# Performance work log

Measured on AMD Instinct MI355X. Metric: run time of the kernel, lower is better.

The kernel has to match this reference:

```python
import jax, jax.numpy as jnp
import numpy as np

# Output volume shape passed as `shape` to forward_3stacks / interpol.grid_push
VOL_SHAPE = (128, 128, 128)


def _grid_push(inp, grid, out_shape):
    """Trilinear scatter-splat (interpol.grid_push, bound=replicate, extrapolate=True).

    inp:  [B, C, D, H, W] values
    grid: [B, D, H, W, 3] target coords in output voxel space, (z, y, x) order
    returns [B, C, *out_shape]
    """
    B, C = inp.shape[0], inp.shape[1]
    S0, S1, S2 = out_shape
    N = inp.shape[2] * inp.shape[3] * inp.shape[4]
    vals = inp.reshape(B, C, N)
    coords = grid.reshape(B, N, 3)

    def push_one(v, g):  # v: [C, N], g: [N, 3]
        g0f = jnp.floor(g)
        f = g - g0f                      # trilinear fractions, [N, 3]
        g0 = g0f.astype(jnp.int32)
        acc = jnp.zeros((C, S0 * S1 * S2), dtype=v.dtype)
        for dz in (0, 1):
            wz = f[:, 0] if dz else 1.0 - f[:, 0]
            iz = jnp.clip(g0[:, 0] + dz, 0, S0 - 1)
            for dy in (0, 1):
                wy = f[:, 1] if dy else 1.0 - f[:, 1]
                iy = jnp.clip(g0[:, 1] + dy, 0, S1 - 1)
                for dx in (0, 1):
                    wx = f[:, 2] if dx else 1.0 - f[:, 2]
                    ix = jnp.clip(g0[:, 2] + dx, 0, S2 - 1)
                    flat = (iz * S1 + iy) * S2 + ix  # [N]
                    w = (wz * wy * wx)[None, :]      # [1, N]
                    acc = acc.at[:, flat].add(v * w)
        return acc.reshape(C, S0, S1, S2)

    return jax.vmap(push_one)(vals, coords)


def setup_inputs() -> dict:
    key = jax.random.key(0)
    k1, k2, k3 = jax.random.split(key, 3)
    x = jax.random.normal(k1, (1, 1, 384, 128, 128), dtype=jnp.float32)
    flow = jax.random.normal(k2, (1, 3, 384, 128, 128), dtype=jnp.float32)
    mask = jax.random.uniform(k3, (1, 1, 384, 128, 128), dtype=jnp.float32)
    return {"x": x, "flow": flow, "mask": mask}


def reference(x, flow, mask):
    """WarpingLayer_3stacks.forward_3stacks with transpose=True, warp=True.

    flow already matches x's spatial shape, so the F.interpolate resize is identity
    (the branch `if flow.shape[2:] != x.shape[2:]` is not taken).
    """
    # per-dim flow rescale: flow[:, d-2] * (x.shape[d]-1)/(flow.shape[d]-1)
    scale = jnp.asarray([(x.shape[d] - 1) / (flow.shape[d] - 1) for d in range(2, 5)],
                        dtype=x.dtype)
    flow = flow * scale[None, :, None, None, None]

    D, H, W = x.shape[2], x.shape[3], x.shape[4]
    gz, gy, gx = jnp.meshgrid(jnp.arange(D, dtype=x.dtype),
                              jnp.arange(H, dtype=x.dtype),
                              jnp.arange(W, dtype=x.dtype), indexing='ij')
    base = jnp.stack([gz, gy, gx], axis=0)          # [3, D, H, W]
    grid = flow + base[None]                        # self.warp * flow + meshgrid
    grid = jnp.transpose(grid, (0, 2, 3, 4, 1))     # [B, D, H, W, 3]

    intensities = jnp.concatenate([x * mask, mask], axis=1)  # [B, 2, D, H, W]
    return _grid_push(intensities, grid, VOL_SHAPE)          # [B, 2, 128, 128, 128]
```

## Files before the change

kernel.cpp:

```cpp
#include <hip/hip_runtime.h>


#define OS    128
#define OS3   (OS * OS * OS)
#define SRC_D 384
#define SRC_H 128
#define SRC_W 128
#define NSRC  (SRC_D * SRC_H * SRC_W)
#define ZSPLIT 128
#define PLANE_CELLS (OS * OS)

#define TZ 8
#define TY 4
#define HALO 3
#define NJOBS 140
#define GITER 9
#define GBLK  512

#define PGROUPS 64
#define PSPB    4
#define PBLK    (PGROUPS * 4)

#define REG_CAP 1024
#define LCAP    65536

#define OFF_CNT    0
#define OFF_COUNTS 1024
#define OFF_REGS   8192
#define OFF_LIST   (OFF_REGS + GBLK * REG_CAP * 16)
#define OFF_PART   (16 * 1024 * 1024)
#define WS_NEED    (OFF_PART + PGROUPS * 2 * PLANE_CELLS * 4)

#define S_FIX   262144.0f
#define INV_FIX (1.0f / 262144.0f)

__device__ __forceinline__ unsigned long long packt(float a, float b) {
    int vi = (int)a;
    int mi = (int)b;
    return ((unsigned long long)(unsigned)vi << 32) | (unsigned long long)(unsigned)mi;
}

__device__ __forceinline__ int swzq(int c) { return c ^ ((c >> 4) & 7); }

__device__ __forceinline__ void atomAddF(float* p, float v) {
    unsafeAtomicAdd(p, v);
}

__global__ __launch_bounds__(512) void warp_fused(
    const float* __restrict__ x, const float* __restrict__ flow,
    const float* __restrict__ mask, float* __restrict__ out,
    float* __restrict__ partials,
    unsigned* __restrict__ gcnt, int* __restrict__ counts,
    int4* __restrict__ regs, int4* __restrict__ list)
{
    __shared__ unsigned long long sh[4096];
    __shared__ int scnt;

    const int tid = threadIdx.x;
    const int b = blockIdx.x;

    const float4* __restrict__ fz4 = (const float4*)flow;
    const float4* __restrict__ fy4 = (const float4*)(flow + NSRC);
    const float4* __restrict__ fx4 = (const float4*)(flow + 2 * NSRC);
    const float4* __restrict__ m4p = (const float4*)mask;
    const float4* __restrict__ x4p = (const float4*)x;

    if (b < GBLK) {
        if (tid == 0) scnt = 0;
        #pragma unroll
        for (int s = 0; s < 4096 / 512; ++s)
            sh[tid + s * 512] = 0ull;
        __syncthreads();

        const int z0 = (b & 15) * TZ;
        const int y0 = (b >> 4) * TY;
        const int wq = tid & 31;
        const int slot = tid >> 5;

        for (int it = 0; it < GITER; ++it) {
            int j = it * 16 + slot;
            int dz = j / 10, dyy = j - dz * 10;
            int zzr = z0 - HALO + dz;
            int hhr = y0 - HALO + dyy;
            int zz = min(max(zzr, 0), ZSPLIT - 1);
            int hh = min(max(hhr, 0), OS - 1);
            bool vrow = (j < NJOBS) && (zzr >= 0) && (zzr < ZSPLIT) &&
                        (hhr >= 0) && (hhr < OS);
            bool home = vrow && (zzr >= z0) && (zzr < z0 + TZ) &&
                        (hhr >= y0) && (hhr < y0 + TY);

            int idx4 = (((zz << 14) + (hh << 7)) >> 2) + wq;
            float4 vfz = fz4[idx4];
            float4 vfy = fy4[idx4];
            float4 vfx = fx4[idx4];
            float4 vm  = m4p[idx4];
            float4 vx  = x4p[idx4];

            if (!vrow) continue;

            #pragma unroll
            for (int p = 0; p < 4; ++p) {
                float gz = ((float*)&vfz)[p] + (float)zz;
                float gy = ((float*)&vfy)[p] + (float)hh;
                float fzf = floorf(gz), fyf = floorf(gy);
                float ffz = gz - fzf, ffy = gy - fyf;
                int iz0 = (int)fzf, iy0 = (int)fyf;

                int cz0 = min(max(iz0,     0), OS - 1);
                int cz1 = min(max(iz0 + 1, 0), OS - 1);
                int cy0 = min(max(iy0,     0), OS - 1);
                int cy1 = min(max(iy0 + 1, 0), OS - 1);

                bool zin = (cz1 >= z0) && (cz0 < z0 + TZ);
                bool yin = (cy1 >= y0) && (cy0 < y0 + TY);
                if (!home && !(zin && yin)) continue;

                int w = wq * 4 + p;
                float gx = ((float*)&vfx)[p] + (float)w;
                float fxf = floorf(gx);
                float ffx = gx - fxf;
                int ix0 = (int)fxf;
                int cx0 = min(max(ix0,     0), OS - 1);
                int cx1 = min(max(ix0 + 1, 0), OS - 1);

                float m = ((float*)&vm)[p];
                float v = ((float*)&vx)[p] * m;
                float v_s = v * S_FIX;
                float m_s = m * S_FIX;

                #pragma unroll
                for (int d2 = 0; d2 < 2; ++d2) {
                    int cz = d2 ? cz1 : cz0;
                    float wz = d2 ? ffz : 1.0f - ffz;
                    bool nz = (cz - zz <= HALO) && (zz - cz <= HALO);
                    int uz = cz - z0;
                    #pragma unroll
                    for (int e2 = 0; e2 < 2; ++e2) {
                        int cy = e2 ? cy1 : cy0;
                        float wzy = wz * (e2 ? ffy : 1.0f - ffy);
                        bool ny = (cy - hh <= HALO) && (hh - cy <= HALO);
                        int uy = cy - y0;
                        bool nearc = nz && ny;
                        #pragma unroll
                        for (int f2 = 0; f2 < 2; ++f2) {
                            int cx = f2 ? cx1 : cx0;
                            float wgt = wzy * (f2 ? ffx : 1.0f - ffx);
                            if (nearc) {
                                if ((unsigned)uz < TZ && (unsigned)uy < TY) {
                                    int off = ((uz * TY + uy) << 7) + swzq(cx);
                                    atomicAdd(&sh[off], packt(v_s * wgt, m_s * wgt));
                                }
                            } else if (home) {
                                int4 r;
                                r.x = (cz << 14) + (cy << 7) + cx;
                                r.y = __float_as_int(v * wgt);
                                r.z = __float_as_int(m * wgt);
                                r.w = 0;
                                int s = atomicAdd(&scnt, 1);
                                if (s < REG_CAP) regs[b * REG_CAP + s] = r;
                                else {
                                    unsigned g = atomicAdd(gcnt, 1u);
                                    if (g < LCAP) list[g] = r;
                                }
                            }
                        }
                    }
                }
            }
        }

        __syncthreads();
        if (tid == 0) counts[b] = min(scnt, REG_CAP);

        for (int i = tid; i < TZ * TY * OS; i += 512) {
            int row = i >> 7;
            int c   = i & 127;
            unsigned long long cell = sh[(row << 7) | swzq(c)];
            float v = (float)(int)(cell >> 32) * INV_FIX;
            float m = (float)(int)(unsigned)cell * INV_FIX;
            int uz = row >> 2, uy = row & 3;
            int o = ((z0 + uz) << 14) + ((y0 + uy) << 7) + c;
            out[o]       = v;
            out[OS3 + o] = m;
        }
    } else {
        const int pb = b - GBLK;
        const int g  = pb >> 2;
        const int q  = pb & 3;
        const int ybase = q << 5;
        const int rlo = max(0, ybase - 5);
        const int rhi = min(OS, ybase + 32 + 5);

        #pragma unroll
        for (int s = 0; s < 4096 / 512; ++s)
            sh[tid + s * 512] = 0ull;
        __syncthreads();

        const int wq = tid & 31;
        const int rs = tid >> 5;

        for (int s = 0; s < PSPB; ++s) {
            int z = ZSPLIT + g * PSPB + s;
            for (int rb = 0; rb < 3; ++rb) {
                int r = rlo + rb * 16 + rs;
                bool valid = r < rhi;
                int rc = min(r, OS - 1);
                int idx4 = (((z << 14) + (rc << 7)) >> 2) + wq;
                float4 vfz = fz4[idx4];
                float4 vfy = fy4[idx4];
                float4 vfx = fx4[idx4];
                float4 vm  = m4p[idx4];
                float4 vx  = x4p[idx4];
                if (!valid) continue;
                bool homeRow = ((r >> 5) == q);

                #pragma unroll
                for (int p = 0; p < 4; ++p) {
                    int w = wq * 4 + p;
                    float gz = ((float*)&vfz)[p] + (float)z;
                    float gy = ((float*)&vfy)[p] + (float)r;
                    float gx = ((float*)&vfx)[p] + (float)w;
                    float m  = ((float*)&vm)[p];
                    float v  = ((float*)&vx)[p] * m;

                    float fyf = floorf(gy), fxf = floorf(gx);
                    float ffy = gy - fyf, ffx = gx - fxf;
                    int iy0 = (int)fyf, ix0 = (int)fxf;
                    int cy0 = min(max(iy0,     0), OS - 1);
                    int cy1 = min(max(iy0 + 1, 0), OS - 1);
                    int cx0 = min(max(ix0,     0), OS - 1);
                    int cx1 = min(max(ix0 + 1, 0), OS - 1);
                    int sx0 = swzq(cx0), sx1 = swzq(cx1);

                    if (gz >= (float)(OS - 1)) {
                        float wy0 = 1.0f - ffy, wy1 = ffy;
                        float wx0 = 1.0f - ffx, wx1 = ffx;
                        float v_s = v * S_FIX;
                        float m_s = m * S_FIX;

                        int u0 = cy0 - ybase;
                        bool n0 = (cy0 - r <= 5) && (r - cy0 <= 5);
                        if (n0 && (unsigned)u0 < 32u) {
                            unsigned long long* row = &sh[u0 << 7];
                            float a = v_s * wy0, bb = m_s * wy0;
                            atomicAdd(&row[sx0], packt(a * wx0, bb * wx0));
                            atomicAdd(&row[sx1], packt(a * wx1, bb * wx1));
                        }
                        int u1 = cy1 - ybase;
                        bool n1 = (cy1 - r <= 5) && (r - cy1 <= 5);
                        if (n1 && (unsigned)u1 < 32u) {
                            unsigned long long* row = &sh[u1 << 7];
                            float a = v_s * wy1, bb = m_s * wy1;
                            atomicAdd(&row[sx0], packt(a * wx0, bb * wx0));
                            atomicAdd(&row[sx1], packt(a * wx1, bb * wx1));
                        }
                        if (homeRow && (!n0 || !n1)) {
                            const int pbase = (OS - 1) << 14;
                            #pragma unroll
                            for (int e2 = 0; e2 < 2; ++e2) {
                                bool far = e2 ? !n1 : !n0;
                                if (!far) continue;
                                int cy = e2 ? cy1 : cy0;
                                float wy = e2 ? wy1 : wy0;
                                unsigned base = atomicAdd(gcnt, 2u);
                                #pragma unroll
                                for (int f2 = 0; f2 < 2; ++f2) {
                                    unsigned slt = base + f2;
                                    if (slt < LCAP) {
                                        float wgt = wy * (f2 ? wx1 : wx0);
                                        int4 qq;
                                        qq.x = pbase + (cy << 7) + (f2 ? cx1 : cx0);
                                        qq.y = __float_as_int(v * wgt);
                                        qq.z = __float_as_int(m * wgt);
                                        qq.w = 0;
                                        list[slt] = qq;
                                    }
                                }
                            }
                        }
                    } else if (homeRow) {
                        float fzf = floorf(gz);
                        float ffz = gz - fzf;
                        int iz0 = (int)fzf;
                        unsigned base = atomicAdd(gcnt, 8u);
                        int t = 0;
                        #pragma unroll
                        for (int d2 = 0; d2 < 2; ++d2) {
                            int cz = min(max(iz0 + d2, 0), OS - 1);
                            float wz = d2 ? ffz : 1.0f - ffz;
                            #pragma unroll
                            for (int e2 = 0; e2 < 2; ++e2) {
                                int cy = e2 ? cy1 : cy0;
                                float wzy = wz * (e2 ? ffy : 1.0f - ffy);
                                #pragma unroll
                                for (int f2 = 0; f2 < 2; ++f2) {
                                    int cx = f2 ? cx1 : cx0;
                                    float wgt = wzy * (f2 ? ffx : 1.0f - ffx);
                                    unsigned slt = base + t;
                                    if (slt < LCAP) {
                                        int4 qq;
                                        qq.x = (cz << 14) + (cy << 7) + cx;
                                        qq.y = __float_as_int(v * wgt);
                                        qq.z = __float_as_int(m * wgt);
                                        qq.w = 0;
                                        list[slt] = qq;
                                    }
                                    ++t;
                                }
                            }
                        }
                    }
                }
            }
        }

        __syncthreads();

        float* dst0 = partials + (size_t)g * 2 * PLANE_CELLS;
        float* dst1 = dst0 + PLANE_CELLS;
        for (int i = tid; i < 32 * OS; i += 512) {
            int row = i >> 7, c = i & 127;
            unsigned long long cell = sh[(row << 7) | swzq(c)];
            float v = (float)(int)(cell >> 32) * INV_FIX;
            float m = (float)(int)(unsigned)cell * INV_FIX;
            int o = ((ybase + row) << 7) + c;
            dst0[o] = v;
            dst1[o] = m;
        }
    }
}

#define RBLK 128
__global__ __launch_bounds__(256) void finalize(
    float* __restrict__ out, const float* __restrict__ partials,
    const unsigned* __restrict__ gcnt, const int* __restrict__ counts,
    const int4* __restrict__ regs, const int4* __restrict__ list)
{
    int b = blockIdx.x;
    if (b < RBLK) {
        int t = b * 256 + threadIdx.x;
        int ch   = t >> 14;
        int cell = t & 16383;
        const float* p = partials + (size_t)ch * PLANE_CELLS + cell;
        float s = 0.0f;
        #pragma unroll 8
        for (int g = 0; g < PGROUPS; ++g)
            s += p[(size_t)g * 2 * PLANE_CELLS];
        atomAddF(out + ch * OS3 + ((OS - 1) << 14) + cell, s);
    } else if (b < RBLK + GBLK) {
        int rb = b - RBLK;
        int n = counts[rb];
        const int4* r = regs + (size_t)rb * REG_CAP;
        for (int i = threadIdx.x; i < n; i += 256) {
            int4 q = r[i];
            atomAddF(out + q.x,       __int_as_float(q.y));
            atomAddF(out + OS3 + q.x, __int_as_float(q.z));
        }
    } else {
        unsigned n = *gcnt;
        if (n > LCAP) n = LCAP;
        for (unsigned i = (unsigned)(b - RBLK - GBLK) * 256 + threadIdx.x;
             i < n; i += 8 * 256) {
            int4 q = list[i];
            atomAddF(out + q.x,       __int_as_float(q.y));
            atomAddF(out + OS3 + q.x, __int_as_float(q.z));
        }
    }
}

__global__ __launch_bounds__(256) void warp_push_naive(
    const float* __restrict__ x, const float* __restrict__ flow,
    const float* __restrict__ mask, float* __restrict__ out, int N)
{
    int idx = blockIdx.x * blockDim.x + threadIdx.x;
    if (idx >= N) return;
    int w = idx & 127, h = (idx >> 7) & 127, z = idx >> 14;
    float gz = flow[idx] + (float)z;
    float gy = flow[N + idx] + (float)h;
    float gx = flow[2 * N + idx] + (float)w;
    float m = mask[idx];
    float v0 = x[idx] * m;
    float fz0 = floorf(gz), fy0 = floorf(gy), fx0 = floorf(gx);
    float fz = gz - fz0, fy = gy - fy0, fx = gx - fx0;
    int iz0 = (int)fz0, iy0 = (int)fy0, ix0 = (int)fx0;
    #pragma unroll
    for (int dz = 0; dz < 2; ++dz) {
        int cz = min(max(iz0 + dz, 0), OS - 1);
        float wz = dz ? fz : 1.0f - fz;
        #pragma unroll
        for (int dy = 0; dy < 2; ++dy) {
            int cy = min(max(iy0 + dy, 0), OS - 1);
            float wzy = wz * (dy ? fy : 1.0f - fy);
            #pragma unroll
            for (int dx = 0; dx < 2; ++dx) {
                int cx = min(max(ix0 + dx, 0), OS - 1);
                float wgt = wzy * (dx ? fx : 1.0f - fx);
                int o = (cz << 14) + (cy << 7) + cx;
                atomAddF(out + o,       v0 * wgt);
                atomAddF(out + OS3 + o, m * wgt);
            }
        }
    }
}

extern "C" void kernel_launch(void* const* d_in, const int* in_sizes, int n_in,
                              void* d_out, int out_size, void* d_ws, size_t ws_size,
                              hipStream_t stream) {
    (void)in_sizes; (void)n_in; (void)out_size;
    const float* x    = (const float*)d_in[0];
    const float* flow = (const float*)d_in[1];
    const float* mask = (const float*)d_in[2];
    float* out = (float*)d_out;

    if (ws_size >= (size_t)WS_NEED) {
        char* wsb = (char*)d_ws;
        unsigned* gcnt = (unsigned*)(wsb + OFF_CNT);
        int* counts    = (int*)(wsb + OFF_COUNTS);
        int4* regs     = (int4*)(wsb + OFF_REGS);
        int4* list     = (int4*)(wsb + OFF_LIST);
        float* parts   = (float*)(wsb + OFF_PART);

        hipMemsetAsync(d_ws, 0, 64, stream);

        warp_fused<<<GBLK + PBLK, 512, 0, stream>>>(
            x, flow, mask, out, parts, gcnt, counts, regs, list);
        finalize<<<RBLK + GBLK + 8, 256, 0, stream>>>(
            out, parts, gcnt, counts, regs, list);
    } else {
        hipMemsetAsync(d_out, 0, (size_t)2 * OS3 * sizeof(float), stream);
        warp_push_naive<<<NSRC / 256, 256, 0, stream>>>(x, flow, mask, out, NSRC);
    }
}
```

Before: 189.6 us.

## Skip halo row loads early and double partial-plane groups

Measured after the change: 200.0 us. 5.5% more time.

```diff
diff --git a/kernel.cpp b/kernel.cpp
--- a/kernel.cpp
+++ b/kernel.cpp
@@ -17,8 +17,8 @@
 #define GITER 9
 #define GBLK  512
 
-#define PGROUPS 64
-#define PSPB    4
+#define PGROUPS 128
+#define PSPB    2
 #define PBLK    (PGROUPS * 4)
 
 #define REG_CAP 1024
@@ -28,7 +28,7 @@
 #define OFF_COUNTS 1024
 #define OFF_REGS   8192
 #define OFF_LIST   (OFF_REGS + GBLK * REG_CAP * 16)
-#define OFF_PART   (16 * 1024 * 1024)
+#define OFF_PART   (10 * 1024 * 1024)
 #define WS_NEED    (OFF_PART + PGROUPS * 2 * PLANE_CELLS * 4)
 
 #define S_FIX   262144.0f
@@ -46,7 +46,7 @@
     unsafeAtomicAdd(p, v);
 }
 
-__global__ __launch_bounds__(512) void warp_fused(
+__global__ __launch_bounds__(512, 8) void warp_fused(
     const float* __restrict__ x, const float* __restrict__ flow,
     const float* __restrict__ mask, float* __restrict__ out,
     float* __restrict__ partials,
@@ -76,6 +76,11 @@
         const int y0 = (b >> 4) * TY;
         const int wq = tid & 31;
         const int slot = tid >> 5;
+
+        const float ztlo = (z0 == 0)           ? -1e30f : (float)(z0 - 1);
+        const float zthi = (z0 + TZ == ZSPLIT) ?  1e30f : (float)(z0 + TZ);
+        const float ytlo = (y0 == 0)           ? -1e30f : (float)(y0 - 1);
+        const float ythi = (y0 + TY == OS)     ?  1e30f : (float)(y0 + TY);
 
         for (int it = 0; it < GITER; ++it) {
             int j = it * 16 + slot;
@@ -92,14 +97,28 @@
             int idx4 = (((zz << 14) + (hh << 7)) >> 2) + wq;
             float4 vfz = fz4[idx4];
             float4 vfy = fy4[idx4];
+            if (!vrow) continue;
+
+            int hitm = 15;
+            if (!home) {
+                hitm = 0;
+                #pragma unroll
+                for (int p = 0; p < 4; ++p) {
+                    float gz = ((float*)&vfz)[p] + (float)zz;
+                    float gy = ((float*)&vfy)[p] + (float)hh;
+                    if (gz >= ztlo && gz < zthi && gy >= ytlo && gy < ythi)
+                        hitm |= 1 << p;
+                }
+                if (hitm == 0) continue;
+            }
+
             float4 vfx = fx4[idx4];
             float4 vm  = m4p[idx4];
             float4 vx  = x4p[idx4];
 
-            if (!vrow) continue;
-
             #pragma unroll
             for (int p = 0; p < 4; ++p) {
+                if (!home && !((hitm >> p) & 1)) continue;
                 float gz = ((float*)&vfz)[p] + (float)zz;
                 float gy = ((float*)&vfy)[p] + (float)hh;
                 float fzf = floorf(gz), fyf = floorf(gy);
@@ -191,6 +210,9 @@
         const int rlo = max(0, ybase - 5);
         const int rhi = min(OS, ybase + 32 + 5);
 
+        const float pylo = (ybase == 0)       ? -1e30f : (float)(ybase - 1);
+        const float pyhi = (ybase + 32 == OS) ?  1e30f : (float)(ybase + 32);
+
         #pragma unroll
         for (int s = 0; s < 4096 / 512; ++s)
             sh[tid + s * 512] = 0ull;
@@ -206,16 +228,29 @@
                 bool valid = r < rhi;
                 int rc = min(r, OS - 1);
                 int idx4 = (((z << 14) + (rc << 7)) >> 2) + wq;
+                float4 vfy = fy4[idx4];
+                if (!valid) continue;
+                bool homeRow = ((r >> 5) == q);
+
+                int hitm = 15;
+                if (!homeRow) {
+                    hitm = 0;
+                    #pragma unroll
+                    for (int p = 0; p < 4; ++p) {
+                        float gy = ((float*)&vfy)[p] + (float)r;
+                        if (gy >= pylo && gy < pyhi) hitm |= 1 << p;
+                    }
+                    if (hitm == 0) continue;
+                }
+
                 float4 vfz = fz4[idx4];
-                float4 vfy = fy4[idx4];
                 float4 vfx = fx4[idx4];
                 float4 vm  = m4p[idx4];
                 float4 vx  = x4p[idx4];
-                if (!valid) continue;
-                bool homeRow = ((r >> 5) == q);
 
                 #pragma unroll
                 for (int p = 0; p < 4; ++p) {
+                    if (!((hitm >> p) & 1)) continue;
                     int w = wq * 4 + p;
                     float gz = ((float*)&vfz)[p] + (float)z;
                     float gy = ((float*)&vfy)[p] + (float)r;
```

## Shrink gather halo and software-prefetch next row loads in both phases

Applied to the files above, without the earlier changes.

Result: slower. 303.8 us (+60.3%).

```diff
diff --git a/kernel.cpp b/kernel.cpp
--- a/kernel.cpp
+++ b/kernel.cpp
@@ -12,16 +12,16 @@
 
 #define TZ 8
 #define TY 4
-#define HALO 3
-#define NJOBS 140
-#define GITER 9
+#define HALO 2
+#define NJOBS 96
+#define GITER 6
 #define GBLK  512
 
 #define PGROUPS 64
 #define PSPB    4
 #define PBLK    (PGROUPS * 4)
 
-#define REG_CAP 1024
+#define REG_CAP 1536
 #define LCAP    65536
 
 #define OFF_CNT    0
@@ -77,24 +77,44 @@
         const int wq = tid & 31;
         const int slot = tid >> 5;
 
-        for (int it = 0; it < GITER; ++it) {
-            int j = it * 16 + slot;
-            int dz = j / 10, dyy = j - dz * 10;
+        float4 nfz, nfy, nfx, nvm, nvx;
+        int nzz, nhh;
+        bool nvrow, nhome;
+        {
+            int j = slot;
+            int dz = j >> 3, dyy = j & 7;
             int zzr = z0 - HALO + dz;
             int hhr = y0 - HALO + dyy;
-            int zz = min(max(zzr, 0), ZSPLIT - 1);
-            int hh = min(max(hhr, 0), OS - 1);
-            bool vrow = (j < NJOBS) && (zzr >= 0) && (zzr < ZSPLIT) &&
+            nzz = min(max(zzr, 0), ZSPLIT - 1);
+            nhh = min(max(hhr, 0), OS - 1);
+            nvrow = (zzr >= 0) && (zzr < ZSPLIT) && (hhr >= 0) && (hhr < OS);
+            nhome = nvrow && (zzr >= z0) && (zzr < z0 + TZ) &&
+                    (hhr >= y0) && (hhr < y0 + TY);
+            int idx4 = (((nzz << 14) + (nhh << 7)) >> 2) + wq;
+            nfz = fz4[idx4]; nfy = fy4[idx4]; nfx = fx4[idx4];
+            nvm = m4p[idx4]; nvx = x4p[idx4];
+        }
+
+        for (int it = 0; it < GITER; ++it) {
+            float4 vfz = nfz, vfy = nfy, vfx = nfx, vm = nvm, vx = nvx;
+            const int zz = nzz, hh = nhh;
+            const bool vrow = nvrow, home = nhome;
+
+            {
+                int j = (it + 1) * 16 + slot;
+                int dz = j >> 3, dyy = j & 7;
+                int zzr = z0 - HALO + dz;
+                int hhr = y0 - HALO + dyy;
+                nzz = min(max(zzr, 0), ZSPLIT - 1);
+                nhh = min(max(hhr, 0), OS - 1);
+                nvrow = (j < NJOBS) && (zzr >= 0) && (zzr < ZSPLIT) &&
                         (hhr >= 0) && (hhr < OS);
-            bool home = vrow && (zzr >= z0) && (zzr < z0 + TZ) &&
+                nhome = nvrow && (zzr >= z0) && (zzr < z0 + TZ) &&
                         (hhr >= y0) && (hhr < y0 + TY);
-
-            int idx4 = (((zz << 14) + (hh << 7)) >> 2) + wq;
-            float4 vfz = fz4[idx4];
-            float4 vfy = fy4[idx4];
-            float4 vfx = fx4[idx4];
-            float4 vm  = m4p[idx4];
-            float4 vx  = x4p[idx4];
+                int idx4 = (((nzz << 14) + (nhh << 7)) >> 2) + wq;
+                nfz = fz4[idx4]; nfy = fy4[idx4]; nfx = fx4[idx4];
+                nvm = m4p[idx4]; nvx = x4p[idx4];
+            }
 
             if (!vrow) continue;
 
@@ -199,114 +219,133 @@
         const int wq = tid & 31;
         const int rs = tid >> 5;
 
-        for (int s = 0; s < PSPB; ++s) {
-            int z = ZSPLIT + g * PSPB + s;
-            for (int rb = 0; rb < 3; ++rb) {
-                int r = rlo + rb * 16 + rs;
-                bool valid = r < rhi;
-                int rc = min(r, OS - 1);
-                int idx4 = (((z << 14) + (rc << 7)) >> 2) + wq;
-                float4 vfz = fz4[idx4];
-                float4 vfy = fy4[idx4];
-                float4 vfx = fx4[idx4];
-                float4 vm  = m4p[idx4];
-                float4 vx  = x4p[idx4];
-                if (!valid) continue;
-                bool homeRow = ((r >> 5) == q);
-
-                #pragma unroll
-                for (int p = 0; p < 4; ++p) {
-                    int w = wq * 4 + p;
-                    float gz = ((float*)&vfz)[p] + (float)z;
-                    float gy = ((float*)&vfy)[p] + (float)r;
-                    float gx = ((float*)&vfx)[p] + (float)w;
-                    float m  = ((float*)&vm)[p];
-                    float v  = ((float*)&vx)[p] * m;
-
-                    float fyf = floorf(gy), fxf = floorf(gx);
-                    float ffy = gy - fyf, ffx = gx - fxf;
-                    int iy0 = (int)fyf, ix0 = (int)fxf;
-                    int cy0 = min(max(iy0,     0), OS - 1);
-                    int cy1 = min(max(iy0 + 1, 0), OS - 1);
-                    int cx0 = min(max(ix0,     0), OS - 1);
-                    int cx1 = min(max(ix0 + 1, 0), OS - 1);
-                    int sx0 = swzq(cx0), sx1 = swzq(cx1);
-
-                    if (gz >= (float)(OS - 1)) {
-                        float wy0 = 1.0f - ffy, wy1 = ffy;
-                        float wx0 = 1.0f - ffx, wx1 = ffx;
-                        float v_s = v * S_FIX;
-                        float m_s = m * S_FIX;
-
-                        int u0 = cy0 - ybase;
-                        bool n0 = (cy0 - r <= 5) && (r - cy0 <= 5);
-                        if (n0 && (unsigned)u0 < 32u) {
-                            unsigned long long* row = &sh[u0 << 7];
-                            float a = v_s * wy0, bb = m_s * wy0;
-                            atomicAdd(&row[sx0], packt(a * wx0, bb * wx0));
-                            atomicAdd(&row[sx1], packt(a * wx1, bb * wx1));
-                        }
-                        int u1 = cy1 - ybase;
-                        bool n1 = (cy1 - r <= 5) && (r - cy1 <= 5);
-                        if (n1 && (unsigned)u1 < 32u) {
-                            unsigned long long* row = &sh[u1 << 7];
-                            float a = v_s * wy1, bb = m_s * wy1;
-                            atomicAdd(&row[sx0], packt(a * wx0, bb * wx0));
-                            atomicAdd(&row[sx1], packt(a * wx1, bb * wx1));
-                        }
-                        if (homeRow && (!n0 || !n1)) {
-                            const int pbase = (OS - 1) << 14;
+        float4 nfz, nfy, nfx, nvm, nvx;
+        int nr, nz;
+        {
+            int r0 = rlo + rs;
+            int rc0 = min(r0, OS - 1);
+            int zp  = ZSPLIT + g * PSPB;
+            int idx4 = (((zp << 14) + (rc0 << 7)) >> 2) + wq;
+            nfz = fz4[idx4]; nfy = fy4[idx4]; nfx = fx4[idx4];
+            nvm = m4p[idx4]; nvx = x4p[idx4];
+            nr = r0; nz = zp;
+        }
+        int cs = 0, crb = 0;
+
+        for (int k = 0; k < PSPB * 3; ++k) {
+            float4 vfz = nfz, vfy = nfy, vfx = nfx, vm = nvm, vx = nvx;
+            const int r = nr;
+            const int z = nz;
+
+            {
+                int krb = (crb == 2) ? 0 : crb + 1;
+                int ks  = (crb == 2) ? cs + 1 : cs;
+                int rn  = rlo + krb * 16 + rs;
+                int zn  = min(ZSPLIT + g * PSPB + ks, SRC_D - 1);
+                int rcn = min(rn, OS - 1);
+                int idx4 = (((zn << 14) + (rcn << 7)) >> 2) + wq;
+                nfz = fz4[idx4]; nfy = fy4[idx4]; nfx = fx4[idx4];
+                nvm = m4p[idx4]; nvx = x4p[idx4];
+                nr = rn; nz = (ks < PSPB) ? zn : z;
+                cs = ks; crb = krb;
+            }
+
+            bool valid = r < rhi;
+            if (!valid) continue;
+            bool homeRow = ((r >> 5) == q);
+
+            #pragma unroll
+            for (int p = 0; p < 4; ++p) {
+                int w = wq * 4 + p;
+                float gz = ((float*)&vfz)[p] + (float)z;
+                float gy = ((float*)&vfy)[p] + (float)r;
+                float gx = ((float*)&vfx)[p] + (float)w;
+                float m  = ((float*)&vm)[p];
+                float v  = ((float*)&vx)[p] * m;
+
+                float fyf = floorf(gy), fxf = floorf(gx);
+                float ffy = gy - fyf, ffx = gx - fxf;
+                int iy0 = (int)fyf, ix0 = (int)fxf;
+                int cy0 = min(max(iy0,     0), OS - 1);
+                int cy1 = min(max(iy0 + 1, 0), OS - 1);
+                int cx0 = min(max(ix0,     0), OS - 1);
+                int cx1 = min(max(ix0 + 1, 0), OS - 1);
+                int sx0 = swzq(cx0), sx1 = swzq(cx1);
+
+                if (gz >= (float)(OS - 1)) {
+                    float wy0 = 1.0f - ffy, wy1 = ffy;
+                    float wx0 = 1.0f - ffx, wx1 = ffx;
+                    float v_s = v * S_FIX;
+                    float m_s = m * S_FIX;
+
+                    int u0 = cy0 - ybase;
+                    bool n0 = (cy0 - r <= 5) && (r - cy0 <= 5);
+                    if (n0 && (unsigned)u0 < 32u) {
+                        unsigned long long* row = &sh[u0 << 7];
+                        float a = v_s * wy0, bb = m_s * wy0;
+                        atomicAdd(&row[sx0], packt(a * wx0, bb * wx0));
+                        atomicAdd(&row[sx1], packt(a * wx1, bb * wx1));
+                    }
+                    int u1 = cy1 - ybase;
+                    bool n1 = (cy1 - r <= 5) && (r - cy1 <= 5);
+                    if (n1 && (unsigned)u1 < 32u) {
+                        unsigned long long* row = &sh[u1 << 7];
+                        float a = v_s * wy1, bb = m_s * wy1;
+                        atomicAdd(&row[sx0], packt(a * wx0, bb * wx0));
+                        atomicAdd(&row[sx1], packt(a * wx1, bb * wx1));
+                    }
+                    if (homeRow && (!n0 || !n1)) {
+                        const int pbase = (OS - 1) << 14;
+                        #pragma unroll
+                        for (int e2 = 0; e2 < 2; ++e2) {
+                            bool far = e2 ? !n1 : !n0;
+                            if (!far) continue;
+                            int cy = e2 ? cy1 : cy0;
+                            float wy = e2 ? wy1 : wy0;
+                            unsigned base = atomicAdd(gcnt, 2u);
                             #pragma unroll
-                            for (int e2 = 0; e2 < 2; ++e2) {
-                                bool far = e2 ? !n1 : !n0;
-                                if (!far) continue;
-                                int cy = e2 ? cy1 : cy0;
-                                float wy = e2 ? wy1 : wy0;
-                                unsigned base = atomicAdd(gcnt, 2u);
-                                #pragma unroll
-                                for (int f2 = 0; f2 < 2; ++f2) {
-                                    unsigned slt = base + f2;
-                                    if (slt < LCAP) {
-                                        float wgt = wy * (f2 ? wx1 : wx0);
-                                        int4 qq;
-                                        qq.x = pbase + (cy << 7) + (f2 ? cx1 : cx0);
-                                        qq.y = __float_as_int(v * wgt);
-                                        qq.z = __float_as_int(m * wgt);
-                                        qq.w = 0;
-                                        list[slt] = qq;
-                                    }
+                            for (int f2 = 0; f2 < 2; ++f2) {
+                                unsigned slt = base + f2;
+                                if (slt < LCAP) {
+                                    float wgt = wy * (f2 ? wx1 : wx0);
+                                    int4 qq;
+                                    qq.x = pbase + (cy << 7) + (f2 ? cx1 : cx0);
+                                    qq.y = __float_as_int(v * wgt);
+                                    qq.z = __float_as_int(m * wgt);
+                                    qq.w = 0;
+                                    list[slt] = qq;
                                 }
                             }
                         }
-                    } else if (homeRow) {
-                        float fzf = floorf(gz);
-                        float ffz = gz - fzf;
-                        int iz0 = (int)fzf;
-                        unsigned base = atomicAdd(gcnt, 8u);
-                        int t = 0;
+                    }
+                } else if (homeRow) {
+                    float fzf = floorf(gz);
+                    float ffz = gz - fzf;
+                    int iz0 = (int)fzf;
+                    unsigned base = atomicAdd(gcnt, 8u);
+                    int t = 0;
+                    #pragma unroll
+                    for (int d2 = 0; d2 < 2; ++d2) {
+                        int cz = min(max(iz0 + d2, 0), OS - 1);
+                        float wz = d2 ? ffz : 1.0f - ffz;
                         #pragma unroll
-                        for (int d2 = 0; d2 < 2; ++d2) {
-                            int cz = min(max(iz0 + d2, 0), OS - 1);
-                            float wz = d2 ? ffz : 1.0f - ffz;
+                        for (int e2 = 0; e2 < 2; ++e2) {
+                            int cy = e2 ? cy1 : cy0;
+                            float wzy = wz * (e2 ? ffy : 1.0f - ffy);
                             #pragma unroll
-                            for (int e2 = 0; e2 < 2; ++e2) {
-                                int cy = e2 ? cy1 : cy0;
-                                float wzy = wz * (e2 ? ffy : 1.0f - ffy);
-                                #pragma unroll
-                                for (int f2 = 0; f2 < 2; ++f2) {
-                                    int cx = f2 ? cx1 : cx0;
-                                    float wgt = wzy * (f2 ? ffx : 1.0f - ffx);
-                                    unsigned slt = base + t;
-                                    if (slt < LCAP) {
-                                        int4 qq;
-                                        qq.x = (cz << 14) + (cy << 7) + cx;
-                                        qq.y = __float_as_int(v * wgt);
-                                        qq.z = __float_as_int(m * wgt);
-                                        qq.w = 0;
-                                        list[slt] = qq;
-                                    }
-                                    ++t;
+                            for (int f2 = 0; f2 < 2; ++f2) {
+                                int cx = f2 ? cx1 : cx0;
+                                float wgt = wzy * (f2 ? ffx : 1.0f - ffx);
+                                unsigned slt = base + t;
+                                if (slt < LCAP) {
+                                    int4 qq;
+                                    qq.x = (cz << 14) + (cy << 7) + cx;
+                                    qq.y = __float_as_int(v * wgt);
+                                    qq.z = __float_as_int(m * wgt);
+                                    qq.w = 0;
+                                    list[slt] = qq;
                                 }
+                                ++t;
                             }
                         }
                     }
```

## Enlarge scatter tiles to 8x8 rows, prefetch next row, use global region counters

Applied to the files above, without the earlier changes.

Measured after the change: 221.1 us. +16.6%, slower.

```diff
diff --git a/kernel.cpp b/kernel.cpp
--- a/kernel.cpp
+++ b/kernel.cpp
@@ -11,11 +11,11 @@
 #define PLANE_CELLS (OS * OS)
 
 #define TZ 8
-#define TY 4
+#define TY 8
 #define HALO 3
-#define NJOBS 140
-#define GITER 9
-#define GBLK  512
+#define NJOBS 196
+#define GITER 13
+#define GBLK  256
 
 #define PGROUPS 64
 #define PSPB    4
@@ -53,9 +53,7 @@
     unsigned* __restrict__ gcnt, int* __restrict__ counts,
     int4* __restrict__ regs, int4* __restrict__ list)
 {
-    __shared__ unsigned long long sh[4096];
-    __shared__ int scnt;
-
+    __shared__ unsigned long long sh[8192];
     const int tid = threadIdx.x;
     const int b = blockIdx.x;
 
@@ -66,9 +64,8 @@
     const float4* __restrict__ x4p = (const float4*)x;
 
     if (b < GBLK) {
-        if (tid == 0) scnt = 0;
         #pragma unroll
-        for (int s = 0; s < 4096 / 512; ++s)
+        for (int s = 0; s < 8192 / 512; ++s)
             sh[tid + s * 512] = 0ull;
         __syncthreads();
 
@@ -77,24 +74,44 @@
         const int wq = tid & 31;
         const int slot = tid >> 5;
 
-        for (int it = 0; it < GITER; ++it) {
-            int j = it * 16 + slot;
-            int dz = j / 10, dyy = j - dz * 10;
+        float4 nfz, nfy, nfx, nvm, nvx;
+        int nzz, nhh;
+        bool nvrow, nhome;
+        {
+            int j = slot;
+            int dz = j / 14, dyy = j - dz * 14;
             int zzr = z0 - HALO + dz;
             int hhr = y0 - HALO + dyy;
-            int zz = min(max(zzr, 0), ZSPLIT - 1);
-            int hh = min(max(hhr, 0), OS - 1);
-            bool vrow = (j < NJOBS) && (zzr >= 0) && (zzr < ZSPLIT) &&
+            nzz = min(max(zzr, 0), ZSPLIT - 1);
+            nhh = min(max(hhr, 0), OS - 1);
+            nvrow = (zzr >= 0) && (zzr < ZSPLIT) && (hhr >= 0) && (hhr < OS);
+            nhome = nvrow && (zzr >= z0) && (zzr < z0 + TZ) &&
+                    (hhr >= y0) && (hhr < y0 + TY);
+            int idx4 = (((nzz << 14) + (nhh << 7)) >> 2) + wq;
+            nfz = fz4[idx4]; nfy = fy4[idx4]; nfx = fx4[idx4];
+            nvm = m4p[idx4]; nvx = x4p[idx4];
+        }
+
+        for (int it = 0; it < GITER; ++it) {
+            float4 vfz = nfz, vfy = nfy, vfx = nfx, vm = nvm, vx = nvx;
+            const int zz = nzz, hh = nhh;
+            const bool vrow = nvrow, home = nhome;
+
+            {
+                int j = (it + 1) * 16 + slot;
+                int dz = j / 14, dyy = j - dz * 14;
+                int zzr = z0 - HALO + dz;
+                int hhr = y0 - HALO + dyy;
+                nzz = min(max(zzr, 0), ZSPLIT - 1);
+                nhh = min(max(hhr, 0), OS - 1);
+                nvrow = (j < NJOBS) && (zzr >= 0) && (zzr < ZSPLIT) &&
                         (hhr >= 0) && (hhr < OS);
-            bool home = vrow && (zzr >= z0) && (zzr < z0 + TZ) &&
+                nhome = nvrow && (zzr >= z0) && (zzr < z0 + TZ) &&
                         (hhr >= y0) && (hhr < y0 + TY);
-
-            int idx4 = (((zz << 14) + (hh << 7)) >> 2) + wq;
-            float4 vfz = fz4[idx4];
-            float4 vfy = fy4[idx4];
-            float4 vfx = fx4[idx4];
-            float4 vm  = m4p[idx4];
-            float4 vx  = x4p[idx4];
+                int idx4 = (((nzz << 14) + (nhh << 7)) >> 2) + wq;
+                nfz = fz4[idx4]; nfy = fy4[idx4]; nfx = fx4[idx4];
+                nvm = m4p[idx4]; nvx = x4p[idx4];
+            }
 
             if (!vrow) continue;
 
@@ -156,7 +173,7 @@
                                 r.y = __float_as_int(v * wgt);
                                 r.z = __float_as_int(m * wgt);
                                 r.w = 0;
-                                int s = atomicAdd(&scnt, 1);
+                                int s = atomicAdd(&counts[b], 1);
                                 if (s < REG_CAP) regs[b * REG_CAP + s] = r;
                                 else {
                                     unsigned g = atomicAdd(gcnt, 1u);
@@ -170,7 +187,6 @@
         }
 
         __syncthreads();
-        if (tid == 0) counts[b] = min(scnt, REG_CAP);
 
         for (int i = tid; i < TZ * TY * OS; i += 512) {
             int row = i >> 7;
@@ -178,7 +194,7 @@
             unsigned long long cell = sh[(row << 7) | swzq(c)];
             float v = (float)(int)(cell >> 32) * INV_FIX;
             float m = (float)(int)(unsigned)cell * INV_FIX;
-            int uz = row >> 2, uy = row & 3;
+            int uz = row >> 3, uy = row & 7;
             int o = ((z0 + uz) << 14) + ((y0 + uy) << 7) + c;
             out[o]       = v;
             out[OS3 + o] = m;
@@ -349,7 +365,7 @@
         atomAddF(out + ch * OS3 + ((OS - 1) << 14) + cell, s);
     } else if (b < RBLK + GBLK) {
         int rb = b - RBLK;
-        int n = counts[rb];
+        int n = min(counts[rb], REG_CAP);
         const int4* r = regs + (size_t)rb * REG_CAP;
         for (int i = threadIdx.x; i < n; i += 256) {
             int4 q = r[i];
@@ -420,7 +436,7 @@
         int4* list     = (int4*)(wsb + OFF_LIST);
         float* parts   = (float*)(wsb + OFF_PART);
 
-        hipMemsetAsync(d_ws, 0, 64, stream);
+        hipMemsetAsync(d_ws, 0, 2048, stream);
 
         warp_fused<<<GBLK + PBLK, 512, 0, stream>>>(
             x, flow, mask, out, parts, gcnt, counts, regs, list);
```
